# Optimization experiments

Measured on AMD Instinct MI355X. Metric: run time of the kernel, lower is better.

## Reference

```python
import jax, jax.numpy as jnp
import numpy as np

N_FEATURES = 1024
N_HEADS = 16
D_ATTN = 64


def setup_inputs() -> dict:
    key = jax.random.key(0)
    k_x, k_qkv, k_pw, k_pb = jax.random.split(key, 4)
    B, S = 2, 2048
    x = jax.random.normal(k_x, (B, S, N_FEATURES), dtype=jnp.float32)
    # torch nn.Linear weights are [out, in]; init scale ~ 1/sqrt(in)
    w_qkv = jax.random.normal(k_qkv, (3 * N_HEADS * D_ATTN, N_FEATURES), dtype=jnp.float32) / np.sqrt(N_FEATURES)
    w_proj = jax.random.normal(k_pw, (N_FEATURES, N_HEADS * D_ATTN), dtype=jnp.float32) / np.sqrt(N_HEADS * D_ATTN)
    b_proj = jax.random.normal(k_pb, (N_FEATURES,), dtype=jnp.float32) / np.sqrt(N_HEADS * D_ATTN)
    return {"x": x, "w_qkv": w_qkv, "w_proj": w_proj, "b_proj": b_proj}


def reference(x, w_qkv, w_proj, b_proj):
    B, S, F = x.shape
    H, D = N_HEADS, D_ATTN
    # fused QKV projection (bias=False): [B,S,3*H*D]
    qkv = jnp.einsum('bsf,of->bso', x, w_qkv)
    qkv = qkv.reshape(B, S, 3, H, D)
    q = jnp.transpose(qkv[:, :, 0], (0, 2, 1, 3))  # [B,H,S,D]
    k = jnp.transpose(qkv[:, :, 1], (0, 2, 1, 3))
    v = jnp.transpose(qkv[:, :, 2], (0, 2, 1, 3))
    scale = 1.0 / jnp.sqrt(jnp.asarray(D, dtype=x.dtype))
    scores = jnp.einsum('bhqd,bhkd->bhqk', q, k) * scale  # [B,H,S,S]
    attn = jax.nn.softmax(scores, axis=-1)
    out = jnp.einsum('bhqk,bhkd->bhqd', attn, v)  # [B,H,S,D]
    out = jnp.transpose(out, (0, 2, 1, 3)).reshape(B, S, H * D)
    # output projection (dropout is identity in eval mode)
    return jnp.einsum('bsm,fm->bsf', out, w_proj) + b_proj
```

## Files before the change

kernel.cpp:

```cpp
#include <hip/hip_runtime.h>
#include <hip/hip_bf16.h>
#include <math.h>

#define BATCH 2
#define SEQ 2048
#define NFEAT 1024
#define NHEAD 16
#define DHEAD 64
#define MROWS (BATCH * SEQ)
#define NQKV (3 * NHEAD * DHEAD)

typedef __attribute__((ext_vector_type(8))) short short8;
typedef __attribute__((ext_vector_type(4))) float floatx4;

__device__ __forceinline__ unsigned short f2bf(float f) {
    unsigned int u = __float_as_uint(f);
    u += 0x7fff + ((u >> 16) & 1);
    return (unsigned short)(u >> 16);
}

__device__ __forceinline__ float fast_exp2(float x) {
    return __builtin_amdgcn_exp2f(x);
}

__device__ __forceinline__ uint pack_bf16x2(float lo, float hi) {
    float2 t; t.x = lo; t.y = hi;
    __hip_bfloat162 h = __float22bfloat162_rn(t);
    union { __hip_bfloat162 h; uint u; } c; c.h = h;
    return c.u;
}

__device__ __forceinline__ void async16(const void* g, void* l) {
    __builtin_amdgcn_global_load_lds(
        (const __attribute__((address_space(1))) void*)g,
        (__attribute__((address_space(3))) void*)l, 16, 0, 0);
}

__global__ void cvt_bf16(const float* __restrict__ in, ushort* __restrict__ out, int n4) {
    int i = blockIdx.x * blockDim.x + threadIdx.x;
    if (i < n4) {
        float4 v = ((const float4*)in)[i];
        ushort4 o;
        o.x = f2bf(v.x); o.y = f2bf(v.y); o.z = f2bf(v.z); o.w = f2bf(v.w);
        ((ushort4*)out)[i] = o;
    }
}

template <int EPI>
__global__ __launch_bounds__(256, 2)
void gemm_bt(const ushort* __restrict__ A, const ushort* __restrict__ W,
             int M, int N, int K,
             ushort* __restrict__ qb, ushort* __restrict__ kb, ushort* __restrict__ vtb,
             const float* __restrict__ bias, float* __restrict__ Cout) {
    __shared__ ushort As[128 * 32];
    __shared__ ushort Bs[128 * 32];
    const int tid = threadIdx.x;
    const int wave = tid >> 6, lane = tid & 63;
    const int m0 = blockIdx.y * 128, n0 = blockIdx.x * 128;
    const int wm = (wave >> 1) * 64, wn = (wave & 1) * 64;
    const int lr = lane & 15, lg = lane >> 4;

    floatx4 acc[4][4] = {};

    const int seg0 = tid, seg1 = tid + 256;
    const int row0 = seg0 >> 2, cb0 = (seg0 & 3) * 8;
    const int row1 = seg1 >> 2, cb1 = (seg1 & 3) * 8;

    for (int k0 = 0; k0 < K; k0 += 32) {
        async16(A + (size_t)(m0 + row0) * K + k0 + cb0, (void*)(As + seg0 * 8));
        async16(A + (size_t)(m0 + row1) * K + k0 + cb1, (void*)(As + seg1 * 8));
        async16(W + (size_t)(n0 + row0) * K + k0 + cb0, (void*)(Bs + seg0 * 8));
        async16(W + (size_t)(n0 + row1) * K + k0 + cb1, (void*)(Bs + seg1 * 8));
        __syncthreads();
        short8 a[4], b[4];
#pragma unroll
        for (int i = 0; i < 4; ++i)
            a[i] = *(const short8*)(As + (wm + i * 16 + lr) * 32 + lg * 8);
#pragma unroll
        for (int j = 0; j < 4; ++j)
            b[j] = *(const short8*)(Bs + (wn + j * 16 + lr) * 32 + lg * 8);
#pragma unroll
        for (int i = 0; i < 4; ++i)
#pragma unroll
            for (int j = 0; j < 4; ++j)
                acc[i][j] = __builtin_amdgcn_mfma_f32_16x16x32_bf16(a[i], b[j], acc[i][j], 0, 0, 0);
        __syncthreads();
    }

#pragma unroll
    for (int i = 0; i < 4; ++i) {
#pragma unroll
        for (int j = 0; j < 4; ++j) {
#pragma unroll
            for (int r = 0; r < 4; ++r) {
                const int m = m0 + wm + i * 16 + lg * 4 + r;
                const int n = n0 + wn + j * 16 + lr;
                const float v = acc[i][j][r];
                if (EPI == 0) {
                    const int bidx = m >> 11, s = m & (SEQ - 1);
                    const int t = n >> 10, rem = n & 1023, h = rem >> 6, d = rem & 63;
                    const ushort bf = f2bf(v);
                    if (t == 2) {
                        const int scol = (s & ~63) | (((((s >> 3) & 7) ^ (d & 7)) << 3)) | (s & 7);
                        vtb[((size_t)(bidx * NHEAD + h) * DHEAD + d) * SEQ + scol] = bf;
                    } else if (t == 1) {
                        const int dcol = ((((d >> 3) ^ (s & 7)) << 3)) | (d & 7);
                        kb[((size_t)(bidx * NHEAD + h) * SEQ + s) * DHEAD + dcol] = bf;
                    } else {
                        qb[((size_t)(bidx * NHEAD + h) * SEQ + s) * DHEAD + d] = bf;
                    }
                } else {
                    Cout[(size_t)m * N + n] = v + bias[n];
                }
            }
        }
    }
}

__global__ __launch_bounds__(256, 4)
void flash_attn(const ushort* __restrict__ qb, const ushort* __restrict__ kb,
                const ushort* __restrict__ vtb, ushort* __restrict__ aob) {
    const int qt = blockIdx.x, bh = blockIdx.y;
    const int tid = threadIdx.x, wave = tid >> 6, lane = tid & 63;
    const int lr = lane & 15, lg = lane >> 4;

    __shared__ ushort Ks[2][64 * 64];
    __shared__ ushort Vs[2][64 * 64];
    __shared__ ushort Ps_all[4][16 * 64];
    ushort* Ps = Ps_all[wave];

    const ushort* Qb = qb + (size_t)bh * SEQ * DHEAD;
    const ushort* Kb = kb + (size_t)bh * SEQ * DHEAD;
    const ushort* Vt = vtb + (size_t)bh * DHEAD * SEQ;

    const int q0 = qt * 64 + wave * 16;

    short8 qf[2];
#pragma unroll
    for (int kk = 0; kk < 2; ++kk)
        qf[kk] = *(const short8*)(Qb + (size_t)(q0 + lr) * DHEAD + kk * 32 + lg * 8);

    {
#pragma unroll
        for (int r = 0; r < 2; ++r)
            async16(Kb + (size_t)(r * 256 + tid) * 8, (void*)(Ks[0] + (r * 256 + tid) * 8));
#pragma unroll
        for (int r = 0; r < 2; ++r)
            async16(Vt + (size_t)(r * 32 + (tid >> 3)) * SEQ + (tid & 7) * 8,
                    (void*)(Vs[0] + (r * 256 + tid) * 8));
    }

    floatx4 acc_o[4] = {};
    float l_lane = 0.0f;
    const float CEXP = 0.125f * 1.44269504f;
    const int sw = lr & 7;

    for (int kt = 0; kt < SEQ / 64; ++kt) {
        const int cur = kt & 1;
        __syncthreads();

        if (kt + 1 < SEQ / 64) {
            const int kv1 = (kt + 1) * 64;
#pragma unroll
            for (int r = 0; r < 2; ++r)
                async16(Kb + (size_t)kv1 * DHEAD + (size_t)(r * 256 + tid) * 8,
                        (void*)(Ks[1 - cur] + (r * 256 + tid) * 8));
#pragma unroll
            for (int r = 0; r < 2; ++r)
                async16(Vt + (size_t)(r * 32 + (tid >> 3)) * SEQ + kv1 + (tid & 7) * 8,
                        (void*)(Vs[1 - cur] + (r * 256 + tid) * 8));
        }

        floatx4 st[4] = {};
#pragma unroll
        for (int kk = 0; kk < 2; ++kk)
#pragma unroll
            for (int i = 0; i < 4; ++i) {
                short8 kf = *(const short8*)(Ks[cur] + (i * 16 + lr) * 64 + (((kk * 4 + lg) ^ sw) * 8));
                st[i] = __builtin_amdgcn_mfma_f32_16x16x32_bf16(kf, qf[kk], st[i], 0, 0, 0);
            }

#pragma unroll
        for (int i = 0; i < 4; ++i) {
            const float p0 = fast_exp2(st[i][0] * CEXP);
            const float p1 = fast_exp2(st[i][1] * CEXP);
            const float p2 = fast_exp2(st[i][2] * CEXP);
            const float p3 = fast_exp2(st[i][3] * CEXP);
            l_lane += (p0 + p1) + (p2 + p3);
            uint2 pk;
            pk.x = pack_bf16x2(p0, p1);
            pk.y = pack_bf16x2(p2, p3);
            const int chunk = i * 2 + (lg >> 1);
            *(uint2*)(Ps + lr * 64 + ((chunk ^ sw) * 8) + (lg & 1) * 4) = pk;
        }

#pragma unroll
        for (int kk2 = 0; kk2 < 2; ++kk2) {
            short8 pf = *(const short8*)(Ps + lr * 64 + (((kk2 * 4 + lg) ^ sw) * 8));
#pragma unroll
            for (int j2 = 0; j2 < 4; ++j2) {
                short8 vf = *(const short8*)(Vs[cur] + (j2 * 16 + lr) * 64 + (((kk2 * 4 + lg) ^ sw) * 8));
                acc_o[j2] = __builtin_amdgcn_mfma_f32_16x16x32_bf16(pf, vf, acc_o[j2], 0, 0, 0);
            }
        }
    }

    l_lane += __shfl_xor(l_lane, 16);
    l_lane += __shfl_xor(l_lane, 32);

    const int b = bh >> 4, h = bh & 15;
#pragma unroll
    for (int r = 0; r < 4; ++r) {
        const float lq = __shfl(l_lane, lg * 4 + r);
        const float invl = 1.0f / lq;
        const int srow = b * SEQ + q0 + lg * 4 + r;
#pragma unroll
        for (int j2 = 0; j2 < 4; ++j2) {
            const int d = j2 * 16 + lr;
            aob[(size_t)srow * (NHEAD * DHEAD) + h * DHEAD + d] = f2bf(acc_o[j2][r] * invl);
        }
    }
}

extern "C" void kernel_launch(void* const* d_in, const int* in_sizes, int n_in,
                              void* d_out, int out_size, void* d_ws, size_t ws_size,
                              hipStream_t stream) {
    const float* x      = (const float*)d_in[0];
    const float* w_qkv  = (const float*)d_in[1];
    const float* w_proj = (const float*)d_in[2];
    const float* b_proj = (const float*)d_in[3];
    float* out = (float*)d_out;

    ushort* ws = (ushort*)d_ws;
    ushort* xb     = ws;
    ushort* wqkvb  = xb + (size_t)MROWS * NFEAT;
    ushort* wprojb = wqkvb + (size_t)NQKV * NFEAT;
    ushort* qb     = wprojb + (size_t)NFEAT * NFEAT;
    ushort* kb     = qb + (size_t)MROWS * NFEAT;
    ushort* vtb    = kb + (size_t)MROWS * NFEAT;
    ushort* aob    = vtb + (size_t)MROWS * NFEAT;

    {
        int n4 = (MROWS * NFEAT) / 4;
        cvt_bf16<<<(n4 + 255) / 256, 256, 0, stream>>>(x, xb, n4);
        n4 = (NQKV * NFEAT) / 4;
        cvt_bf16<<<(n4 + 255) / 256, 256, 0, stream>>>(w_qkv, wqkvb, n4);
        n4 = (NFEAT * NFEAT) / 4;
        cvt_bf16<<<(n4 + 255) / 256, 256, 0, stream>>>(w_proj, wprojb, n4);
    }

    {
        dim3 grid(NQKV / 128, MROWS / 128);
        gemm_bt<0><<<grid, 256, 0, stream>>>(xb, wqkvb, MROWS, NQKV, NFEAT,
                                             qb, kb, vtb, nullptr, nullptr);
    }

    {
        dim3 grid(SEQ / 64, BATCH * NHEAD);
        flash_attn<<<grid, 256, 0, stream>>>(qb, kb, vtb, aob);
    }

    {
        dim3 grid(NFEAT / 128, MROWS / 128);
        gemm_bt<1><<<grid, 256, 0, stream>>>(aob, wprojb, MROWS, NFEAT, NFEAT,
                                             nullptr, nullptr, nullptr, b_proj, out);
    }
}
```

Measured before the change: 206.5 us.

## Swizzle GEMM operands, fold softmax scale into Q, stage V transpose through LDS

Merges the three bf16 conversion kernels into one launch that writes K-dimension-swizzled layouts, so the GEMM LDS fragment reads avoid bank conflicts. The attention output is written with the same swizzle for the projection GEMM. The QKV epilogue folds the softmax scale and log2e into Q and writes V transposed through shared memory with 16-byte stores instead of scattered 2-byte stores. The flash kernel loop is manually unrolled by two with fixed buffer indices, removing the per-element scale multiply. Rounding Q after scaling changes numerics slightly, and the added LDS staging adds barriers in the epilogue.

```diff
diff --git a/kernel.cpp b/kernel.cpp
--- a/kernel.cpp
+++ b/kernel.cpp
@@ -13,6 +13,8 @@
 typedef __attribute__((ext_vector_type(8))) short short8;
 typedef __attribute__((ext_vector_type(4))) float floatx4;
 
+#define CEXP 0.18033688f
+
 __device__ __forceinline__ unsigned short f2bf(float f) {
     unsigned int u = __float_as_uint(f);
     u += 0x7fff + ((u >> 16) & 1);
@@ -36,14 +38,25 @@
         (__attribute__((address_space(3))) void*)l, 16, 0, 0);
 }
 
-__global__ void cvt_bf16(const float* __restrict__ in, ushort* __restrict__ out, int n4) {
+__global__ void cvt_swz(const float* __restrict__ x, const float* __restrict__ wq,
+                        const float* __restrict__ wp,
+                        ushort* __restrict__ xb, ushort* __restrict__ wqb,
+                        ushort* __restrict__ wpb) {
+    const int NX = MROWS * NFEAT / 4, NWQ = NQKV * NFEAT / 4, NWP = NFEAT * NFEAT / 4;
     int i = blockIdx.x * blockDim.x + threadIdx.x;
-    if (i < n4) {
-        float4 v = ((const float4*)in)[i];
-        ushort4 o;
-        o.x = f2bf(v.x); o.y = f2bf(v.y); o.z = f2bf(v.z); o.w = f2bf(v.w);
-        ((ushort4*)out)[i] = o;
-    }
+    if (i >= NX + NWQ + NWP) return;
+    const float* src; ushort* dst; int idx4;
+    if (i < NX)            { src = x;  dst = xb;  idx4 = i; }
+    else if (i < NX + NWQ) { src = wq; dst = wqb; idx4 = i - NX; }
+    else                   { src = wp; dst = wpb; idx4 = i - NX - NWQ; }
+    float4 v = ((const float4*)src)[idx4];
+    ushort4 o;
+    o.x = f2bf(v.x); o.y = f2bf(v.y); o.z = f2bf(v.z); o.w = f2bf(v.w);
+    const int e = idx4 * 4;
+    const int k = e & (NFEAT - 1);
+    const int row = e >> 10;
+    const int kp = (k & ~31) | (((((k >> 3) & 3) ^ ((row >> 1) & 3))) << 3) | (k & 7);
+    *(ushort4*)(dst + (size_t)row * NFEAT + kp) = o;
 }
 
 template <int EPI>
@@ -52,13 +65,15 @@
              int M, int N, int K,
              ushort* __restrict__ qb, ushort* __restrict__ kb, ushort* __restrict__ vtb,
              const float* __restrict__ bias, float* __restrict__ Cout) {
-    __shared__ ushort As[128 * 32];
-    __shared__ ushort Bs[128 * 32];
+    __shared__ ushort smem[8192];
+    ushort* As = smem;
+    ushort* Bs = smem + 4096;
     const int tid = threadIdx.x;
     const int wave = tid >> 6, lane = tid & 63;
     const int m0 = blockIdx.y * 128, n0 = blockIdx.x * 128;
     const int wm = (wave >> 1) * 64, wn = (wave & 1) * 64;
     const int lr = lane & 15, lg = lane >> 4;
+    const int kswz = (lg ^ ((lr >> 1) & 3)) * 8;
 
     floatx4 acc[4][4] = {};
 
@@ -75,10 +90,10 @@
         short8 a[4], b[4];
 #pragma unroll
         for (int i = 0; i < 4; ++i)
-            a[i] = *(const short8*)(As + (wm + i * 16 + lr) * 32 + lg * 8);
+            a[i] = *(const short8*)(As + (wm + i * 16 + lr) * 32 + kswz);
 #pragma unroll
         for (int j = 0; j < 4; ++j)
-            b[j] = *(const short8*)(Bs + (wn + j * 16 + lr) * 32 + lg * 8);
+            b[j] = *(const short8*)(Bs + (wn + j * 16 + lr) * 32 + kswz);
 #pragma unroll
         for (int i = 0; i < 4; ++i)
 #pragma unroll
@@ -87,32 +102,71 @@
         __syncthreads();
     }
 
-#pragma unroll
-    for (int i = 0; i < 4; ++i) {
-#pragma unroll
-        for (int j = 0; j < 4; ++j) {
-#pragma unroll
-            for (int r = 0; r < 4; ++r) {
-                const int m = m0 + wm + i * 16 + lg * 4 + r;
-                const int n = n0 + wn + j * 16 + lr;
-                const float v = acc[i][j][r];
-                if (EPI == 0) {
-                    const int bidx = m >> 11, s = m & (SEQ - 1);
-                    const int t = n >> 10, rem = n & 1023, h = rem >> 6, d = rem & 63;
-                    const ushort bf = f2bf(v);
-                    if (t == 2) {
-                        const int scol = (s & ~63) | (((((s >> 3) & 7) ^ (d & 7)) << 3)) | (s & 7);
-                        vtb[((size_t)(bidx * NHEAD + h) * DHEAD + d) * SEQ + scol] = bf;
-                    } else if (t == 1) {
+    if (EPI == 1) {
+#pragma unroll
+        for (int i = 0; i < 4; ++i)
+#pragma unroll
+            for (int j = 0; j < 4; ++j)
+#pragma unroll
+                for (int r = 0; r < 4; ++r) {
+                    const int m = m0 + wm + i * 16 + lg * 4 + r;
+                    const int n = n0 + wn + j * 16 + lr;
+                    Cout[(size_t)m * N + n] = acc[i][j][r] + bias[n];
+                }
+        return;
+    }
+
+    const int t = n0 >> 10;
+    const int bidx = m0 >> 11;
+    if (t < 2) {
+#pragma unroll
+        for (int i = 0; i < 4; ++i)
+#pragma unroll
+            for (int j = 0; j < 4; ++j)
+#pragma unroll
+                for (int r = 0; r < 4; ++r) {
+                    const int m = m0 + wm + i * 16 + lg * 4 + r;
+                    const int n = n0 + wn + j * 16 + lr;
+                    const int s = m & (SEQ - 1);
+                    const int rem = n & 1023, h = rem >> 6, d = rem & 63;
+                    if (t == 0) {
+                        qb[((size_t)(bidx * NHEAD + h) * SEQ + s) * DHEAD + d] =
+                            f2bf(acc[i][j][r] * CEXP);
+                    } else {
                         const int dcol = ((((d >> 3) ^ (s & 7)) << 3)) | (d & 7);
-                        kb[((size_t)(bidx * NHEAD + h) * SEQ + s) * DHEAD + dcol] = bf;
-                    } else {
-                        qb[((size_t)(bidx * NHEAD + h) * SEQ + s) * DHEAD + d] = bf;
+                        kb[((size_t)(bidx * NHEAD + h) * SEQ + s) * DHEAD + dcol] =
+                            f2bf(acc[i][j][r]);
                     }
-                } else {
-                    Cout[(size_t)m * N + n] = v + bias[n];
+                }
+    } else {
+#pragma unroll
+        for (int hhalf = 0; hhalf < 2; ++hhalf) {
+            if ((wm >> 6) == hhalf) {
+#pragma unroll
+                for (int i = 0; i < 4; ++i) {
+                    const int chunk = i * 2 + (lg >> 1);
+#pragma unroll
+                    for (int j = 0; j < 4; ++j) {
+                        const int n = wn + j * 16 + lr;
+                        uint2 pk;
+                        pk.x = pack_bf16x2(acc[i][j][0], acc[i][j][1]);
+                        pk.y = pack_bf16x2(acc[i][j][2], acc[i][j][3]);
+                        *(uint2*)(smem + n * 64 + ((chunk ^ (n & 7)) * 8) + (lg & 1) * 4) = pk;
+                    }
                 }
             }
+            __syncthreads();
+            const int s_base = (m0 & (SEQ - 1)) + hhalf * 64;
+#pragma unroll
+            for (int it = 0; it < 4; ++it) {
+                const int n_r = (tid >> 3) + it * 32;
+                const int p = tid & 7;
+                short8 rowv = *(const short8*)(smem + n_r * 64 + p * 8);
+                const int nglob = n0 + n_r;
+                const int d = nglob & 63, hh = (nglob & 1023) >> 6;
+                *(short8*)(vtb + ((size_t)(bidx * NHEAD + hh) * DHEAD + d) * SEQ + s_base + p * 8) = rowv;
+            }
+            __syncthreads();
         }
     }
 }
@@ -140,70 +194,75 @@
     for (int kk = 0; kk < 2; ++kk)
         qf[kk] = *(const short8*)(Qb + (size_t)(q0 + lr) * DHEAD + kk * 32 + lg * 8);
 
-    {
-#pragma unroll
-        for (int r = 0; r < 2; ++r)
-            async16(Kb + (size_t)(r * 256 + tid) * 8, (void*)(Ks[0] + (r * 256 + tid) * 8));
-#pragma unroll
-        for (int r = 0; r < 2; ++r)
-            async16(Vt + (size_t)(r * 32 + (tid >> 3)) * SEQ + (tid & 7) * 8,
-                    (void*)(Vs[0] + (r * 256 + tid) * 8));
-    }
+    const int kofs = tid * 8;
+    const size_t vrow = (size_t)(tid >> 3) * SEQ;
+    const int vcol = (tid & 7) * 8;
+
+    async16(Kb + kofs,                    (void*)(Ks[0] + kofs));
+    async16(Kb + 2048 + kofs,             (void*)(Ks[0] + 2048 + kofs));
+    async16(Vt + vrow + vcol,             (void*)(Vs[0] + kofs));
+    async16(Vt + 32 * SEQ + vrow + vcol,  (void*)(Vs[0] + 2048 + kofs));
 
     floatx4 acc_o[4] = {};
     float l_lane = 0.0f;
-    const float CEXP = 0.125f * 1.44269504f;
     const int sw = lr & 7;
 
-    for (int kt = 0; kt < SEQ / 64; ++kt) {
-        const int cur = kt & 1;
+#define FLASH_PREFETCH(BUF, KV)                                                     \
+    {                                                                               \
+        const int kv_ = (KV);                                                       \
+        async16(Kb + (size_t)kv_ * DHEAD + kofs,          (void*)(Ks[BUF] + kofs)); \
+        async16(Kb + (size_t)kv_ * DHEAD + 2048 + kofs,   (void*)(Ks[BUF] + 2048 + kofs)); \
+        async16(Vt + vrow + kv_ + vcol,                   (void*)(Vs[BUF] + kofs)); \
+        async16(Vt + 32 * SEQ + vrow + kv_ + vcol,        (void*)(Vs[BUF] + 2048 + kofs)); \
+    }
+
+#define FLASH_COMPUTE(BUF)                                                          \
+    {                                                                               \
+        floatx4 st[4] = {};                                                         \
+        _Pragma("unroll")                                                           \
+        for (int kk = 0; kk < 2; ++kk)                                              \
+            _Pragma("unroll")                                                       \
+            for (int i = 0; i < 4; ++i) {                                           \
+                short8 kf = *(const short8*)(Ks[BUF] + (i * 16 + lr) * 64 +         \
+                                             (((kk * 4 + lg) ^ sw) * 8));           \
+                st[i] = __builtin_amdgcn_mfma_f32_16x16x32_bf16(kf, qf[kk], st[i], 0, 0, 0); \
+            }                                                                       \
+        _Pragma("unroll")                                                           \
+        for (int i = 0; i < 4; ++i) {                                               \
+            const float p0 = fast_exp2(st[i][0]);                                   \
+            const float p1 = fast_exp2(st[i][1]);                                   \
+            const float p2 = fast_exp2(st[i][2]);                                   \
+            const float p3 = fast_exp2(st[i][3]);                                   \
+            l_lane += (p0 + p1) + (p2 + p3);                                        \
+            uint2 pk;                                                               \
+            pk.x = pack_bf16x2(p0, p1);                                             \
+            pk.y = pack_bf16x2(p2, p3);                                             \
+            const int chunk = i * 2 + (lg >> 1);                                    \
+            *(uint2*)(Ps + lr * 64 + ((chunk ^ sw) * 8) + (lg & 1) * 4) = pk;       \
+        }                                                                           \
+        _Pragma("unroll")                                                           \
+        for (int kk2 = 0; kk2 < 2; ++kk2) {                                         \
+            short8 pf = *(const short8*)(Ps + lr * 64 + (((kk2 * 4 + lg) ^ sw) * 8)); \
+            _Pragma("unroll")                                                       \
+            for (int j2 = 0; j2 < 4; ++j2) {                                        \
+                short8 vf = *(const short8*)(Vs[BUF] + (j2 * 16 + lr) * 64 +        \
+                                             (((kk2 * 4 + lg) ^ sw) * 8));          \
+                acc_o[j2] = __builtin_amdgcn_mfma_f32_16x16x32_bf16(pf, vf, acc_o[j2], 0, 0, 0); \
+            }                                                                       \
+        }                                                                           \
+    }
+
+    for (int kt = 0; kt < SEQ / 64; kt += 2) {
         __syncthreads();
-
-        if (kt + 1 < SEQ / 64) {
-            const int kv1 = (kt + 1) * 64;
-#pragma unroll
-            for (int r = 0; r < 2; ++r)
-                async16(Kb + (size_t)kv1 * DHEAD + (size_t)(r * 256 + tid) * 8,
-                        (void*)(Ks[1 - cur] + (r * 256 + tid) * 8));
-#pragma unroll
-            for (int r = 0; r < 2; ++r)
-                async16(Vt + (size_t)(r * 32 + (tid >> 3)) * SEQ + kv1 + (tid & 7) * 8,
-                        (void*)(Vs[1 - cur] + (r * 256 + tid) * 8));
-        }
-
-        floatx4 st[4] = {};
-#pragma unroll
-        for (int kk = 0; kk < 2; ++kk)
-#pragma unroll
-            for (int i = 0; i < 4; ++i) {
-                short8 kf = *(const short8*)(Ks[cur] + (i * 16 + lr) * 64 + (((kk * 4 + lg) ^ sw) * 8));
-                st[i] = __builtin_amdgcn_mfma_f32_16x16x32_bf16(kf, qf[kk], st[i], 0, 0, 0);
-            }
-
-#pragma unroll
-        for (int i = 0; i < 4; ++i) {
-            const float p0 = fast_exp2(st[i][0] * CEXP);
-            const float p1 = fast_exp2(st[i][1] * CEXP);
-            const float p2 = fast_exp2(st[i][2] * CEXP);
-            const float p3 = fast_exp2(st[i][3] * CEXP);
-            l_lane += (p0 + p1) + (p2 + p3);
-            uint2 pk;
-            pk.x = pack_bf16x2(p0, p1);
-            pk.y = pack_bf16x2(p2, p3);
-            const int chunk = i * 2 + (lg >> 1);
-            *(uint2*)(Ps + lr * 64 + ((chunk ^ sw) * 8) + (lg & 1) * 4) = pk;
-        }
-
-#pragma unroll
-        for (int kk2 = 0; kk2 < 2; ++kk2) {
-            short8 pf = *(const short8*)(Ps + lr * 64 + (((kk2 * 4 + lg) ^ sw) * 8));
-#pragma unroll
-            for (int j2 = 0; j2 < 4; ++j2) {
-                short8 vf = *(const short8*)(Vs[cur] + (j2 * 16 + lr) * 64 + (((kk2 * 4 + lg) ^ sw) * 8));
-                acc_o[j2] = __builtin_amdgcn_mfma_f32_16x16x32_bf16(pf, vf, acc_o[j2], 0, 0, 0);
-            }
-        }
-    }
+        FLASH_PREFETCH(1, (kt + 1) * 64)
+        FLASH_COMPUTE(0)
+        __syncthreads();
+        if (kt + 2 < SEQ / 64)
+            FLASH_PREFETCH(0, (kt + 2) * 64)
+        FLASH_COMPUTE(1)
+    }
+#undef FLASH_PREFETCH
+#undef FLASH_COMPUTE
 
     l_lane += __shfl_xor(l_lane, 16);
     l_lane += __shfl_xor(l_lane, 32);
@@ -214,10 +273,12 @@
         const float lq = __shfl(l_lane, lg * 4 + r);
         const float invl = 1.0f / lq;
         const int srow = b * SEQ + q0 + lg * 4 + r;
+        const int key = (srow >> 1) & 3;
 #pragma unroll
         for (int j2 = 0; j2 < 4; ++j2) {
             const int d = j2 * 16 + lr;
-            aob[(size_t)srow * (NHEAD * DHEAD) + h * DHEAD + d] = f2bf(acc_o[j2][r] * invl);
+            const int dsw = (d & ~31) | (((((d >> 3) & 3) ^ key)) << 3) | (d & 7);
+            aob[(size_t)srow * (NHEAD * DHEAD) + h * DHEAD + dsw] = f2bf(acc_o[j2][r] * invl);
         }
     }
 }
@@ -241,12 +302,8 @@
     ushort* aob    = vtb + (size_t)MROWS * NFEAT;
 
     {
-        int n4 = (MROWS * NFEAT) / 4;
-        cvt_bf16<<<(n4 + 255) / 256, 256, 0, stream>>>(x, xb, n4);
-        n4 = (NQKV * NFEAT) / 4;
-        cvt_bf16<<<(n4 + 255) / 256, 256, 0, stream>>>(w_qkv, wqkvb, n4);
-        n4 = (NFEAT * NFEAT) / 4;
-        cvt_bf16<<<(n4 + 255) / 256, 256, 0, stream>>>(w_proj, wprojb, n4);
+        const int total = (MROWS * NFEAT + NQKV * NFEAT + NFEAT * NFEAT) / 4;
+        cvt_swz<<<(total + 255) / 256, 256, 0, stream>>>(x, w_qkv, w_proj, xb, wqkvb, wprojb);
     }
 
     {
```

Result: faster. 194.2 us (-5.9%).
